# Performance work log

Measured on AMD Instinct MI355X. Metric: run time of the kernel, lower is better.

Reference implementation:

```python
import jax, jax.numpy as jnp
import numpy as np

N_NODE = 50000
N_EDGE = 800000
D = 64       # in_dim = out_dim = hidden_dim
A = 64       # attn_dim
N_REL = 475  # 2*237+1 relation ids
B = 32       # batch of queries


def setup_inputs() -> dict:
    key = jax.random.key(0)
    ks = jax.random.split(key, 16)
    hidden = jax.random.normal(ks[0], (N_NODE, D), dtype=jnp.float32)
    sub = jax.random.randint(ks[1], (N_EDGE,), 0, N_NODE)
    rel = jax.random.randint(ks[2], (N_EDGE,), 0, N_REL)
    obj = jax.random.randint(ks[3], (N_EDGE,), 0, N_NODE)
    edges = jnp.stack([sub, rel, obj], axis=1)  # [E, 3]
    gnn_emb_rel = jax.random.normal(ks[4], (N_REL, D), dtype=jnp.float32)
    mapping = jax.random.randint(ks[5], (N_REL,), 0, N_REL)  # rel id -> unique-rel row
    q_rel = jax.random.randint(ks[6], (B,), 0, N_REL)
    r_idx = jax.random.randint(ks[7], (N_EDGE,), 0, B)  # edge -> query index
    s = 1.0 / np.sqrt(D)
    sa = 1.0 / np.sqrt(A)
    u = lambda k, shape, b: jax.random.uniform(k, shape, jnp.float32, minval=-b, maxval=b)
    return {
        "hidden": hidden,
        "edges": edges,
        "gnn_emb_rel": gnn_emb_rel,
        "mapping": mapping,
        "q_rel": q_rel,
        "r_idx": r_idx,
        "n_node": N_NODE,
        "Ws_w": u(ks[8], (A, D), s),
        "Wr_w": u(ks[9], (A, D), s),
        "Wqr_w": u(ks[10], (A, D), s),
        "Wqr_b": u(ks[11], (A,), s),
        "walpha_w": u(ks[12], (1, A), sa),
        "walpha_b": u(ks[13], (1,), sa),
        "Wh_w": u(ks[14], (D, D), s),
    }


def reference(hidden, edges, gnn_emb_rel, mapping, q_rel, r_idx, n_node,
              Ws_w, Wr_w, Wqr_w, Wqr_b, walpha_w, walpha_b, Wh_w):
    sub, rel, obj = edges[:, 0], edges[:, 1], edges[:, 2]
    hs = hidden[sub]                       # [E, D] gather
    hr = gnn_emb_rel[mapping[rel]]         # [E, D] gather
    # per-query h_qr projected once, then gathered per edge (same math, cheaper)
    hq = gnn_emb_rel[mapping[q_rel]]       # [B, D]
    qr_attn = hq @ Wqr_w.T + Wqr_b         # [B, A]
    pre = hs @ Ws_w.T + hr @ Wr_w.T + qr_attn[r_idx]   # [E, A]
    alpha = jax.nn.sigmoid(jax.nn.relu(pre) @ walpha_w.T + walpha_b)  # [E, 1]
    message = alpha * (hs * hr)            # [E, D]
    message_agg = jax.ops.segment_sum(message, obj, num_segments=n_node)  # [N, D]
    hidden_new = jax.nn.relu(message_agg @ Wh_w.T)  # act = ReLU from GNN_auto
    return hidden_new
```

## Files before the change

kernel.cpp:

```cpp
#include <hip/hip_runtime.h>
#include <hip/hip_bf16.h>

#define D64 64
#define WTP 65
#define LPAD 72

typedef __attribute__((ext_vector_type(8))) short short8;
typedef __attribute__((ext_vector_type(4))) float f32x4;

__device__ inline float lane_bcast(float v, int l) {
    return __uint_as_float(__builtin_amdgcn_readlane(__float_as_uint(v), l));
}
__device__ inline float bf16_lo(unsigned u) { return __uint_as_float(u << 16); }
__device__ inline float bf16_hi(unsigned u) { return __uint_as_float(u & 0xFFFF0000u); }
__device__ inline float bf16u(unsigned short u) { return __uint_as_float((unsigned)u << 16); }
__device__ inline unsigned short f2bf(float f) {
    __hip_bfloat16 b = __float2bfloat16(f);
    return *(unsigned short*)&b;
}

__global__ void cvtW_kernel(const float* __restrict__ W, unsigned short* __restrict__ WsB) {
    int i = blockIdx.x * blockDim.x + threadIdx.x;
    if (i < D64 * D64) WsB[i] = f2bf(W[i]);
}

__global__ void rowmm_mfma_kernel(const float* __restrict__ in,
                                  const unsigned short* __restrict__ WsB,
                                  unsigned short* __restrict__ outb,
                                  unsigned short* __restrict__ inb, int nrows) {
    __shared__ unsigned short ldsA[4][16 * LPAD];
    int tid = threadIdx.x;
    int lane = tid & 63;
    int wv = tid >> 6;
    int wid = (blockIdx.x * blockDim.x + tid) >> 6;
    int rbase = wid * 16;
    if (rbase >= nrows) return;

    short8 bfrag[8];
#pragma unroll
    for (int t = 0; t < 4; ++t)
#pragma unroll
        for (int kk = 0; kk < 2; ++kk)
            bfrag[t * 2 + kk] = *(const short8*)(WsB + (size_t)(t * 16 + (lane & 15)) * D64 +
                                                 kk * 32 + (lane >> 4) * 8);

    unsigned short* la = &ldsA[wv][0];
#pragma unroll
    for (int rr = 0; rr < 16; ++rr) {
        float v = in[(size_t)(rbase + rr) * D64 + lane];
        unsigned short b = f2bf(v);
        inb[(size_t)(rbase + rr) * D64 + lane] = b;
        la[rr * LPAD + lane] = b;
    }

    f32x4 acc[4];
#pragma unroll
    for (int t = 0; t < 4; ++t) acc[t] = (f32x4){0.f, 0.f, 0.f, 0.f};
#pragma unroll
    for (int kk = 0; kk < 2; ++kk) {
        short8 afrag = *(const short8*)(la + (lane & 15) * LPAD + kk * 32 + (lane >> 4) * 8);
#pragma unroll
        for (int t = 0; t < 4; ++t)
            acc[t] = __builtin_amdgcn_mfma_f32_16x16x32_bf16(afrag, bfrag[t * 2 + kk],
                                                             acc[t], 0, 0, 0);
    }
#pragma unroll
    for (int t = 0; t < 4; ++t)
#pragma unroll
        for (int reg = 0; reg < 4; ++reg) {
            int row = rbase + (lane >> 4) * 4 + reg;
            int col = t * 16 + (lane & 15);
            outb[(size_t)row * D64 + col] = f2bf(acc[t][reg]);
        }
}

__global__ void hist_pack_kernel(const int* __restrict__ edges, const int* __restrict__ r_idx,
                                 int* __restrict__ counts, uint2* __restrict__ epack, int E) {
    int gt = blockIdx.x * blockDim.x + threadIdx.x;
    int gs = gridDim.x * blockDim.x;
    for (int i = gt; i < E; i += gs) {
        int sub = edges[i * 3 + 0];
        int rel = edges[i * 3 + 1];
        int obj = edges[i * 3 + 2];
        int ri  = r_idx[i];
        epack[i] = make_uint2((unsigned)sub | ((unsigned)rel << 17) | ((unsigned)ri << 26),
                              (unsigned)obj);
        atomicAdd(&counts[obj], 1);
    }
}

__global__ void prep_kernel(const float* __restrict__ emb, const int* __restrict__ mapping,
                            const int* __restrict__ q_rel,
                            const float* __restrict__ Wr, const float* __restrict__ Wqr,
                            const float* __restrict__ Wqr_b,
                            unsigned short* __restrict__ hrmapb,
                            unsigned short* __restrict__ hrWb,
                            unsigned short* __restrict__ qrb, int nrel, int nq) {
    int b = blockIdx.x;
    int lane = threadIdx.x;
    if (b < nrel) {
        int m = mapping[b];
        float v = emb[m * D64 + lane];
        hrmapb[b * D64 + lane] = f2bf(v);
        float acc = 0.f;
#pragma unroll
        for (int d = 0; d < D64; ++d)
            acc = fmaf(lane_bcast(v, d), Wr[lane * D64 + d], acc);
        hrWb[b * D64 + lane] = f2bf(acc);
    } else {
        int q = b - nrel;
        if (q < nq) {
            int m = mapping[q_rel[q]];
            float v = emb[m * D64 + lane];
            float acc = Wqr_b[lane];
#pragma unroll
            for (int d = 0; d < D64; ++d)
                acc = fmaf(lane_bcast(v, d), Wqr[lane * D64 + d], acc);
            qrb[q * D64 + lane] = f2bf(acc);
        }
    }
}

__global__ void scan1_kernel(const int* __restrict__ counts, int* __restrict__ offs,
                             int* __restrict__ partials, int n) {
    __shared__ int tsum[256];
    int t = threadIdx.x;
    int base = blockIdx.x * 1024 + t * 4;
    int v[4];
    int s = 0;
#pragma unroll
    for (int i = 0; i < 4; ++i) {
        int idx = base + i;
        int c = (idx < n) ? counts[idx] : 0;
        v[i] = s;
        s += c;
    }
    tsum[t] = s;
    __syncthreads();
    for (int off = 1; off < 256; off <<= 1) {
        int y = (t >= off) ? tsum[t - off] : 0;
        __syncthreads();
        tsum[t] += y;
        __syncthreads();
    }
    int incl = tsum[t];
    int thread_prefix = incl - s;
    if (t == 255) partials[blockIdx.x] = incl;
#pragma unroll
    for (int i = 0; i < 4; ++i) {
        int idx = base + i;
        if (idx < n) offs[idx] = thread_prefix + v[i];
    }
}

__global__ void scan2_kernel(int* partials, int nb) {
    int t = threadIdx.x;
    int own = (t < nb) ? partials[t] : 0;
    int v = own;
    for (int off = 1; off < 64; off <<= 1) {
        int y = __shfl_up(v, off, 64);
        if (t >= off) v += y;
    }
    if (t < nb) partials[t] = v - own;
}

__global__ void scan3_kernel(int* __restrict__ offs, const int* __restrict__ partials, int n) {
    int base = blockIdx.x * 1024 + threadIdx.x;
    int add = partials[blockIdx.x];
#pragma unroll
    for (int i = 0; i < 4; ++i) {
        int idx = base + i * 256;
        if (idx < n) offs[idx] += add;
    }
}

__global__ void alpha_scatter_kernel(const uint2* __restrict__ epack,
                                     const unsigned short* __restrict__ hsWb,
                                     const unsigned short* __restrict__ hrWb,
                                     const unsigned short* __restrict__ qrb,
                                     const float* __restrict__ walpha_w,
                                     const float* __restrict__ walpha_b,
                                     int* __restrict__ offs, int2* __restrict__ rec,
                                     int E, int half) {
    int tid = blockIdx.x * blockDim.x + threadIdx.x;
    int e0 = tid >> 3;
    int l = tid & 7;
    if (e0 >= half) return;
    int e1 = e0 + half;
    bool has1 = (e1 < E);

    uint2 p0 = epack[e0];
    uint2 p1 = has1 ? epack[e1] : make_uint2(0u, 0u);
    int sub0 = p0.x & 0x1FFFF, rel0 = (p0.x >> 17) & 0x1FF, ri0 = p0.x >> 26, obj0 = (int)p0.y;
    int sub1 = p1.x & 0x1FFFF, rel1 = (p1.x >> 17) & 0x1FF, ri1 = p1.x >> 26, obj1 = (int)p1.y;

    uint4 hv0 = *(const uint4*)(hsWb + (size_t)sub0 * D64 + l * 8);
    uint4 rv0 = *(const uint4*)(hrWb + (size_t)rel0 * D64 + l * 8);
    uint4 qv0 = *(const uint4*)(qrb  + (size_t)ri0  * D64 + l * 8);
    uint4 hv1 = *(const uint4*)(hsWb + (size_t)sub1 * D64 + l * 8);
    uint4 rv1 = *(const uint4*)(hrWb + (size_t)rel1 * D64 + l * 8);
    uint4 qv1 = *(const uint4*)(qrb  + (size_t)ri1  * D64 + l * 8);
    const float4* w = (const float4*)(walpha_w + l * 8);
    float4 w0 = w[0], w1 = w[1];

    float x0, x1;
    x0 = fmaxf(bf16_lo(hv0.x) + bf16_lo(rv0.x) + bf16_lo(qv0.x), 0.f) * w0.x;
    x0 = fmaf(fmaxf(bf16_hi(hv0.x) + bf16_hi(rv0.x) + bf16_hi(qv0.x), 0.f), w0.y, x0);
    x0 = fmaf(fmaxf(bf16_lo(hv0.y) + bf16_lo(rv0.y) + bf16_lo(qv0.y), 0.f), w0.z, x0);
    x0 = fmaf(fmaxf(bf16_hi(hv0.y) + bf16_hi(rv0.y) + bf16_hi(qv0.y), 0.f), w0.w, x0);
    x0 = fmaf(fmaxf(bf16_lo(hv0.z) + bf16_lo(rv0.z) + bf16_lo(qv0.z), 0.f), w1.x, x0);
    x0 = fmaf(fmaxf(bf16_hi(hv0.z) + bf16_hi(rv0.z) + bf16_hi(qv0.z), 0.f), w1.y, x0);
    x0 = fmaf(fmaxf(bf16_lo(hv0.w) + bf16_lo(rv0.w) + bf16_lo(qv0.w), 0.f), w1.z, x0);
    x0 = fmaf(fmaxf(bf16_hi(hv0.w) + bf16_hi(rv0.w) + bf16_hi(qv0.w), 0.f), w1.w, x0);

    x1 = fmaxf(bf16_lo(hv1.x) + bf16_lo(rv1.x) + bf16_lo(qv1.x), 0.f) * w0.x;
    x1 = fmaf(fmaxf(bf16_hi(hv1.x) + bf16_hi(rv1.x) + bf16_hi(qv1.x), 0.f), w0.y, x1);
    x1 = fmaf(fmaxf(bf16_lo(hv1.y) + bf16_lo(rv1.y) + bf16_lo(qv1.y), 0.f), w0.z, x1);
    x1 = fmaf(fmaxf(bf16_hi(hv1.y) + bf16_hi(rv1.y) + bf16_hi(qv1.y), 0.f), w0.w, x1);
    x1 = fmaf(fmaxf(bf16_lo(hv1.z) + bf16_lo(rv1.z) + bf16_lo(qv1.z), 0.f), w1.x, x1);
    x1 = fmaf(fmaxf(bf16_hi(hv1.z) + bf16_hi(rv1.z) + bf16_hi(qv1.z), 0.f), w1.y, x1);
    x1 = fmaf(fmaxf(bf16_lo(hv1.w) + bf16_lo(rv1.w) + bf16_lo(qv1.w), 0.f), w1.z, x1);
    x1 = fmaf(fmaxf(bf16_hi(hv1.w) + bf16_hi(rv1.w) + bf16_hi(qv1.w), 0.f), w1.w, x1);

    x0 += __shfl_xor(x0, 4, 64);
    x1 += __shfl_xor(x1, 4, 64);
    x0 += __shfl_xor(x0, 2, 64);
    x1 += __shfl_xor(x1, 2, 64);
    x0 += __shfl_xor(x0, 1, 64);
    x1 += __shfl_xor(x1, 1, 64);

    if (l == 0) {
        float wb = walpha_b[0];
        float a0 = 1.f / (1.f + __expf(-(x0 + wb)));
        int slot0 = atomicAdd(&offs[obj0], 1);
        rec[slot0] = make_int2(sub0 | (rel0 << 17), __float_as_int(a0));
        if (has1) {
            float a1 = 1.f / (1.f + __expf(-(x1 + wb)));
            int slot1 = atomicAdd(&offs[obj1], 1);
            rec[slot1] = make_int2(sub1 | (rel1 << 17), __float_as_int(a1));
        }
    }
}

__global__ void agg_wh_kernel(const int2* __restrict__ rec, const int* __restrict__ endoff,
                              const unsigned short* __restrict__ hiddenb,
                              const unsigned short* __restrict__ hrmapb,
                              const float* __restrict__ Wh,
                              float* __restrict__ out, int NN) {
    __shared__ float WT[D64 * WTP];
    int tid = threadIdx.x;
    for (int i = tid; i < D64 * D64; i += blockDim.x)
        WT[(i & 63) * WTP + (i >> 6)] = Wh[i];
    __syncthreads();
    int lane = tid & 63;
    int n = (blockIdx.x * blockDim.x + tid) >> 6;
    if (n >= NN) return;
    int start = (n == 0) ? 0 : endoff[n - 1];
    int end = endoff[n];
    start = __builtin_amdgcn_readfirstlane(start);
    end = __builtin_amdgcn_readfirstlane(end);
    float acc0 = 0.f, acc1 = 0.f, acc2 = 0.f, acc3 = 0.f;
    for (int base = start; base < end; base += 64) {
        int cnt = end - base;
        if (cnt > 64) cnt = 64;
        int rx = 0, ry = 0;
        if (lane < cnt) {
            int2 r = rec[base + lane];
            rx = r.x; ry = r.y;
        }
        int j = 0;
        for (; j + 3 < cnt; j += 4) {
            int rx0 = __builtin_amdgcn_readlane(rx, j);
            int ry0 = __builtin_amdgcn_readlane(ry, j);
            int rx1 = __builtin_amdgcn_readlane(rx, j + 1);
            int ry1 = __builtin_amdgcn_readlane(ry, j + 1);
            int rx2 = __builtin_amdgcn_readlane(rx, j + 2);
            int ry2 = __builtin_amdgcn_readlane(ry, j + 2);
            int rx3 = __builtin_amdgcn_readlane(rx, j + 3);
            int ry3 = __builtin_amdgcn_readlane(ry, j + 3);
            float h0 = bf16u(hiddenb[(size_t)(rx0 & 0x1FFFF) * D64 + lane]);
            float m0 = bf16u(hrmapb[(size_t)((unsigned)rx0 >> 17) * D64 + lane]);
            float h1 = bf16u(hiddenb[(size_t)(rx1 & 0x1FFFF) * D64 + lane]);
            float m1 = bf16u(hrmapb[(size_t)((unsigned)rx1 >> 17) * D64 + lane]);
            float h2 = bf16u(hiddenb[(size_t)(rx2 & 0x1FFFF) * D64 + lane]);
            float m2 = bf16u(hrmapb[(size_t)((unsigned)rx2 >> 17) * D64 + lane]);
            float h3 = bf16u(hiddenb[(size_t)(rx3 & 0x1FFFF) * D64 + lane]);
            float m3 = bf16u(hrmapb[(size_t)((unsigned)rx3 >> 17) * D64 + lane]);
            acc0 = fmaf(__uint_as_float(ry0) * h0, m0, acc0);
            acc1 = fmaf(__uint_as_float(ry1) * h1, m1, acc1);
            acc2 = fmaf(__uint_as_float(ry2) * h2, m2, acc2);
            acc3 = fmaf(__uint_as_float(ry3) * h3, m3, acc3);
        }
        for (; j < cnt; ++j) {
            int rx0 = __builtin_amdgcn_readlane(rx, j);
            int ry0 = __builtin_amdgcn_readlane(ry, j);
            float h0 = bf16u(hiddenb[(size_t)(rx0 & 0x1FFFF) * D64 + lane]);
            float m0 = bf16u(hrmapb[(size_t)((unsigned)rx0 >> 17) * D64 + lane]);
            acc0 = fmaf(__uint_as_float(ry0) * h0, m0, acc0);
        }
    }
    float acc = (acc0 + acc1) + (acc2 + acc3);
    float o = 0.f;
#pragma unroll
    for (int d = 0; d < D64; ++d)
        o = fmaf(lane_bcast(acc, d), WT[d * WTP + lane], o);
    out[(size_t)n * D64 + lane] = fmaxf(o, 0.f);
}

extern "C" void kernel_launch(void* const* d_in, const int* in_sizes, int n_in,
                              void* d_out, int out_size, void* d_ws, size_t ws_size,
                              hipStream_t stream) {
    const float* hidden   = (const float*)d_in[0];
    const int*   edges    = (const int*)d_in[1];
    const float* emb_rel  = (const float*)d_in[2];
    const int*   mapping  = (const int*)d_in[3];
    const int*   q_rel    = (const int*)d_in[4];
    const int*   r_idx    = (const int*)d_in[5];
    const float* Ws_w     = (const float*)d_in[7];
    const float* Wr_w     = (const float*)d_in[8];
    const float* Wqr_w    = (const float*)d_in[9];
    const float* Wqr_b    = (const float*)d_in[10];
    const float* walpha_w = (const float*)d_in[11];
    const float* walpha_b = (const float*)d_in[12];
    const float* Wh_w     = (const float*)d_in[13];
    float* out = (float*)d_out;

    int NN   = in_sizes[0] / D64;
    int E    = in_sizes[5];
    int NREL = in_sizes[3];
    int NQ   = in_sizes[4];

    char* ws = (char*)d_ws;
    size_t off = 0;
    unsigned short* hsWb    = (unsigned short*)(ws + off); off += (size_t)NN * D64 * 2;
    unsigned short* hiddenb = (unsigned short*)(ws + off); off += (size_t)NN * D64 * 2;
    int2*  rec  = (int2*)(ws + off);       off += (size_t)E * sizeof(int2);
    uint2* epack = (uint2*)(ws + off);     off += (size_t)E * sizeof(uint2);
    int* counts = (int*)(ws + off);        off += (size_t)NN * sizeof(int);
    int* offs   = (int*)(ws + off);        off += (size_t)NN * sizeof(int);
    int* partials = (int*)(ws + off);      off += 64 * sizeof(int);
    unsigned short* hrmapb = (unsigned short*)(ws + off); off += (size_t)NREL * D64 * 2;
    unsigned short* hrWb   = (unsigned short*)(ws + off); off += (size_t)NREL * D64 * 2;
    unsigned short* qrb    = (unsigned short*)(ws + off); off += (size_t)NQ * D64 * 2;
    unsigned short* WsB    = (unsigned short*)(ws + off); off += (size_t)D64 * D64 * 2;

    int NB = (NN + 1023) / 1024;

    hipMemsetAsync(counts, 0, (size_t)NN * sizeof(int), stream);
    cvtW_kernel<<<(D64 * D64 + 255) / 256, 256, 0, stream>>>(Ws_w, WsB);
    prep_kernel<<<NREL + NQ, 64, 0, stream>>>(emb_rel, mapping, q_rel, Wr_w, Wqr_w, Wqr_b,
                                              hrmapb, hrWb, qrb, NREL, NQ);
    {
        int waves = (NN + 15) / 16;
        int blocks = (waves * 64 + 255) / 256;
        rowmm_mfma_kernel<<<blocks, 256, 0, stream>>>(hidden, WsB, hsWb, hiddenb, NN);
    }
    hist_pack_kernel<<<2048, 256, 0, stream>>>(edges, r_idx, counts, epack, E);
    scan1_kernel<<<NB, 256, 0, stream>>>(counts, offs, partials, NN);
    scan2_kernel<<<1, 64, 0, stream>>>(partials, NB);
    scan3_kernel<<<NB, 256, 0, stream>>>(offs, partials, NN);
    {
        int half = (E + 1) / 2;
        long long threads = (long long)half * 8;
        int blocks = (int)((threads + 255) / 256);
        alpha_scatter_kernel<<<blocks, 256, 0, stream>>>(epack, hsWb, hrWb, qrb,
                                                         walpha_w, walpha_b, offs, rec, E, half);
    }
    agg_wh_kernel<<<(NN * 64 + 1023) / 1024, 1024, 0, stream>>>(rec, offs, hiddenb, hrmapb,
                                                                Wh_w, out, NN);
}
```

Before: 157.2 us.

## Fuse edge histogram/pack into row matmul kernel and vectorize bf16 stores via LDS

Merges the edge packing and per-object histogram pass into the hidden-row MFMA projection kernel, which removes one kernel launch and lets both independent workloads share the same grid. The bf16 copies of the input rows and of the projection outputs are now staged through LDS and written as 16-byte row stores instead of scattered 2-byte stores. The LDS row pad changes from 72 to 68, and partial 16-row tiles are now guarded. The histogram loop now runs with the matmul grid size rather than 2048 blocks, which changes its per-thread work and raises LDS use per block.

```diff
diff --git a/kernel.cpp b/kernel.cpp
--- a/kernel.cpp
+++ b/kernel.cpp
@@ -3,7 +3,7 @@
 
 #define D64 64
 #define WTP 65
-#define LPAD 72
+#define LPAD 68
 
 typedef __attribute__((ext_vector_type(8))) short short8;
 typedef __attribute__((ext_vector_type(4))) float f32x4;
@@ -27,56 +27,72 @@
 __global__ void rowmm_mfma_kernel(const float* __restrict__ in,
                                   const unsigned short* __restrict__ WsB,
                                   unsigned short* __restrict__ outb,
-                                  unsigned short* __restrict__ inb, int nrows) {
+                                  unsigned short* __restrict__ inb, int nrows,
+                                  const int* __restrict__ edges, const int* __restrict__ r_idx,
+                                  int* __restrict__ counts, uint2* __restrict__ epack, int E) {
     __shared__ unsigned short ldsA[4][16 * LPAD];
+    __shared__ unsigned short ldsD[4][16 * LPAD];
     int tid = threadIdx.x;
     int lane = tid & 63;
     int wv = tid >> 6;
     int wid = (blockIdx.x * blockDim.x + tid) >> 6;
     int rbase = wid * 16;
-    if (rbase >= nrows) return;
-
-    short8 bfrag[8];
-#pragma unroll
-    for (int t = 0; t < 4; ++t)
-#pragma unroll
-        for (int kk = 0; kk < 2; ++kk)
-            bfrag[t * 2 + kk] = *(const short8*)(WsB + (size_t)(t * 16 + (lane & 15)) * D64 +
-                                                 kk * 32 + (lane >> 4) * 8);
-
-    unsigned short* la = &ldsA[wv][0];
-#pragma unroll
-    for (int rr = 0; rr < 16; ++rr) {
-        float v = in[(size_t)(rbase + rr) * D64 + lane];
-        unsigned short b = f2bf(v);
-        inb[(size_t)(rbase + rr) * D64 + lane] = b;
-        la[rr * LPAD + lane] = b;
-    }
-
-    f32x4 acc[4];
-#pragma unroll
-    for (int t = 0; t < 4; ++t) acc[t] = (f32x4){0.f, 0.f, 0.f, 0.f};
-#pragma unroll
-    for (int kk = 0; kk < 2; ++kk) {
-        short8 afrag = *(const short8*)(la + (lane & 15) * LPAD + kk * 32 + (lane >> 4) * 8);
+
+    if (rbase < nrows) {
+        short8 bfrag[8];
 #pragma unroll
         for (int t = 0; t < 4; ++t)
-            acc[t] = __builtin_amdgcn_mfma_f32_16x16x32_bf16(afrag, bfrag[t * 2 + kk],
-                                                             acc[t], 0, 0, 0);
-    }
-#pragma unroll
-    for (int t = 0; t < 4; ++t)
-#pragma unroll
-        for (int reg = 0; reg < 4; ++reg) {
-            int row = rbase + (lane >> 4) * 4 + reg;
-            int col = t * 16 + (lane & 15);
-            outb[(size_t)row * D64 + col] = f2bf(acc[t][reg]);
-        }
-}
-
-__global__ void hist_pack_kernel(const int* __restrict__ edges, const int* __restrict__ r_idx,
-                                 int* __restrict__ counts, uint2* __restrict__ epack, int E) {
-    int gt = blockIdx.x * blockDim.x + threadIdx.x;
+#pragma unroll
+            for (int kk = 0; kk < 2; ++kk)
+                bfrag[t * 2 + kk] = *(const short8*)(WsB + (size_t)(t * 16 + (lane & 15)) * D64 +
+                                                     kk * 32 + (lane >> 4) * 8);
+
+        unsigned short* la = &ldsA[wv][0];
+#pragma unroll
+        for (int rr = 0; rr < 16; ++rr) {
+            int r = rbase + rr;
+            float v = (r < nrows) ? in[(size_t)r * D64 + lane] : 0.f;
+            la[rr * LPAD + lane] = f2bf(v);
+        }
+#pragma unroll
+        for (int h = 0; h < 2; ++h) {
+            int row = h * 8 + (lane >> 3);
+            int col8 = (lane & 7) * 8;
+            if (rbase + row < nrows) {
+                uint4 v = *(const uint4*)(la + row * LPAD + col8);
+                *(uint4*)(inb + (size_t)(rbase + row) * D64 + col8) = v;
+            }
+        }
+
+        f32x4 acc[4];
+#pragma unroll
+        for (int t = 0; t < 4; ++t) acc[t] = (f32x4){0.f, 0.f, 0.f, 0.f};
+#pragma unroll
+        for (int kk = 0; kk < 2; ++kk) {
+            short8 afrag = *(const short8*)(la + (lane & 15) * LPAD + kk * 32 + (lane >> 4) * 8);
+#pragma unroll
+            for (int t = 0; t < 4; ++t)
+                acc[t] = __builtin_amdgcn_mfma_f32_16x16x32_bf16(afrag, bfrag[t * 2 + kk],
+                                                                 acc[t], 0, 0, 0);
+        }
+        unsigned short* ld = &ldsD[wv][0];
+#pragma unroll
+        for (int t = 0; t < 4; ++t)
+#pragma unroll
+            for (int reg = 0; reg < 4; ++reg)
+                ld[((lane >> 4) * 4 + reg) * LPAD + t * 16 + (lane & 15)] = f2bf(acc[t][reg]);
+#pragma unroll
+        for (int h = 0; h < 2; ++h) {
+            int row = h * 8 + (lane >> 3);
+            int col8 = (lane & 7) * 8;
+            if (rbase + row < nrows) {
+                uint4 v = *(const uint4*)(ld + row * LPAD + col8);
+                *(uint4*)(outb + (size_t)(rbase + row) * D64 + col8) = v;
+            }
+        }
+    }
+
+    int gt = blockIdx.x * blockDim.x + tid;
     int gs = gridDim.x * blockDim.x;
     for (int i = gt; i < E; i += gs) {
         int sub = edges[i * 3 + 0];
@@ -353,9 +369,9 @@
     {
         int waves = (NN + 15) / 16;
         int blocks = (waves * 64 + 255) / 256;
-        rowmm_mfma_kernel<<<blocks, 256, 0, stream>>>(hidden, WsB, hsWb, hiddenb, NN);
-    }
-    hist_pack_kernel<<<2048, 256, 0, stream>>>(edges, r_idx, counts, epack, E);
+        rowmm_mfma_kernel<<<blocks, 256, 0, stream>>>(hidden, WsB, hsWb, hiddenb, NN,
+                                                      edges, r_idx, counts, epack, E);
+    }
     scan1_kernel<<<NB, 256, 0, stream>>>(counts, offs, partials, NN);
     scan2_kernel<<<1, 64, 0, stream>>>(partials, NB);
     scan3_kernel<<<NB, 256, 0, stream>>>(offs, partials, NN);
```

After: 154.2 us. No clear change (-1.9%).
